# Optimization experiments

Measured on AMD Instinct MI355X. Metric: run time of the kernel, lower is better.

The kernel has to match this reference:

```python
import jax, jax.numpy as jnp
import numpy as np

HIDDEN = 2048
Q_HEADS = 16
KV_HEADS = 4
HEAD_DIM = HIDDEN // Q_HEADS  # 128
GROUPS = Q_HEADS // KV_HEADS  # 4


def setup_inputs() -> dict:
    key = jax.random.key(0)
    ks = jax.random.split(key, 5)
    scale = 1.0 / np.sqrt(HIDDEN)
    x = jax.random.normal(ks[0], (1, 4096, HIDDEN), dtype=jnp.float32)
    # nn.Linear weights stored as [out_features, in_features]
    Wq = jax.random.uniform(ks[1], (Q_HEADS * HEAD_DIM, HIDDEN), jnp.float32, -scale, scale)
    Wk = jax.random.uniform(ks[2], (KV_HEADS * HEAD_DIM, HIDDEN), jnp.float32, -scale, scale)
    Wv = jax.random.uniform(ks[3], (KV_HEADS * HEAD_DIM, HIDDEN), jnp.float32, -scale, scale)
    Wo = jax.random.uniform(ks[4], (HIDDEN, HIDDEN), jnp.float32, -scale, scale)
    return {"x": x, "Wq": Wq, "Wk": Wk, "Wv": Wv, "Wo": Wo}


def reference(x, Wq, Wk, Wv, Wo):
    b, s, _ = x.shape
    norm = jnp.asarray(np.sqrt(HEAD_DIM), x.dtype)
    # Projections (Linear without bias: x @ W.T)
    q = (x @ Wq.T).reshape(b, s, KV_HEADS, GROUPS, HEAD_DIM)  # group q heads by shared kv head
    k = (x @ Wk.T).reshape(b, s, KV_HEADS, HEAD_DIM)
    v = (x @ Wv.T).reshape(b, s, KV_HEADS, HEAD_DIM)
    # Scores: repeat_interleave of KV is equivalent to sharing k across the g axis
    att = jnp.einsum('bskgd,btkd->bkgst', q, k) / norm  # [b,kv,groups,s,s]
    att = jax.nn.softmax(att, axis=-1)
    out = jnp.einsum('bkgst,btkd->bskgd', att, v).reshape(b, s, HIDDEN)
    return out @ Wo.T
```

## Files before the change

kernel.cpp:

```cpp
#include <hip/hip_runtime.h>
#include <stdint.h>

#define SEQ 4096
#define HID 2048

typedef __attribute__((ext_vector_type(8))) short short8;
typedef __attribute__((ext_vector_type(4))) float f32x4;
typedef __attribute__((ext_vector_type(16))) float f32x16;
typedef unsigned int u32;
typedef __attribute__((ext_vector_type(4))) u32 u32x4;

__device__ __forceinline__ short bf16_rne(float f) {
  u32 u = __builtin_bit_cast(u32, f);
  u += 0x7FFFu + ((u >> 16) & 1u);
  return (short)(u >> 16);
}

__device__ __forceinline__ void gload16(const void* gp, void* lp) {
  __builtin_amdgcn_global_load_lds(
      (const __attribute__((address_space(1))) u32*)(uintptr_t)gp,
      (__attribute__((address_space(3))) u32*)(uintptr_t)lp, 16, 0, 0);
}

__global__ __launch_bounds__(256) void cast_bf16(const float* __restrict__ in,
                                                 short* __restrict__ out, int n8,
                                                 float scale) {
  int i = blockIdx.x * 256 + threadIdx.x;
  if (i >= n8) return;
  const f32x4* p = (const f32x4*)in + (size_t)i * 2;
  f32x4 a = p[0], b = p[1];
  short8 o;
#pragma unroll
  for (int j = 0; j < 4; ++j) { o[j] = bf16_rne(a[j] * scale); o[j + 4] = bf16_rne(b[j] * scale); }
  *((short8*)out + i) = o;
}

__global__ __launch_bounds__(256) void transpose_v(const short* __restrict__ qkv,
                                                   short* __restrict__ vt) {
  __shared__ __align__(16) short tile[64][72];
  int rb = blockIdx.x * 64, cb = blockIdx.y * 64;
  int tid = threadIdx.x;
  int tr = tid >> 3, tc = (tid & 7) * 8;
#pragma unroll
  for (int i = 0; i < 2; ++i)
    *(short8*)&tile[tr + i * 32][tc] =
        *(const short8*)&qkv[(size_t)(rb + tr + i * 32) * 3072 + 2560 + cb + tc];
  __syncthreads();
#pragma unroll
  for (int i = 0; i < 2; ++i) {
    int c = tr + i * 32;
    short8 v;
#pragma unroll
    for (int j = 0; j < 8; ++j) {
      int pos = tc + j;
      int tl = (pos & ~15) | (pos & 3) | ((pos & 4) << 1) | ((pos & 8) >> 1);
      v[j] = tile[tl][c];
    }
    *(short8*)&vt[(size_t)(cb + c) * SEQ + rb + tc] = v;
  }
}

template <typename CT>
__global__ __launch_bounds__(256, 2) void gemm_nt(const short* __restrict__ A,
                                                  const short* __restrict__ B,
                                                  CT* __restrict__ C, int M, int N, int K) {
  __shared__ __align__(16) short As[128 * 32];
  __shared__ __align__(16) short Bs[128 * 32];
  int tid = threadIdx.x, wave = tid >> 6, lane = tid & 63;
  int lr = lane & 15, lg = lane >> 4;
  int wr = wave >> 1, wc = wave & 1;
  size_t rowA0 = (size_t)blockIdx.y * 128, colB0 = (size_t)blockIdx.x * 128;
  f32x4 acc[4][4] = {};

  for (int kt = 0; kt < K; kt += 32) {
#pragma unroll
    for (int c = 0; c < 2; ++c) {
      int chunk = wave * 2 + c;
      int row = chunk * 16 + (lane >> 2);
      int col = (lane & 3) * 8;
      gload16(A + (rowA0 + row) * (size_t)K + kt + col, &As[chunk * 512]);
      gload16(B + (colB0 + row) * (size_t)K + kt + col, &Bs[chunk * 512]);
    }
    __syncthreads();
    short8 a[4], b[4];
#pragma unroll
    for (int i = 0; i < 4; ++i) {
      a[i] = *(const short8*)&As[(wr * 64 + i * 16 + lr) * 32 + lg * 8];
      b[i] = *(const short8*)&Bs[(wc * 64 + i * 16 + lr) * 32 + lg * 8];
    }
#pragma unroll
    for (int i = 0; i < 4; ++i)
#pragma unroll
      for (int j = 0; j < 4; ++j)
        acc[i][j] = __builtin_amdgcn_mfma_f32_16x16x32_bf16(a[i], b[j], acc[i][j], 0, 0, 0);
    __syncthreads();
  }
#pragma unroll
  for (int i = 0; i < 4; ++i)
#pragma unroll
    for (int j = 0; j < 4; ++j)
#pragma unroll
      for (int r = 0; r < 4; ++r) {
        size_t row = rowA0 + wr * 64 + i * 16 + lg * 4 + r;
        size_t col = colB0 + wc * 64 + j * 16 + lr;
        if constexpr (sizeof(CT) == 2) C[row * N + col] = (CT)bf16_rne(acc[i][j][r]);
        else C[row * N + col] = acc[i][j][r];
      }
}

__global__ __launch_bounds__(256, 2) void attn_kernel(const short* __restrict__ QKV,
                                                      const short* __restrict__ Vt,
                                                      short* __restrict__ Oat) {
  __shared__ __align__(16) short Ks[2][4096];
  __shared__ __align__(16) short Vs[2][4096];
  int tid = threadIdx.x, wave = tid >> 6, lane = tid & 63;
  int l31 = lane & 31, hi = lane >> 5;
  int h = blockIdx.y, kv = h >> 2;
  int q0 = blockIdx.x * 128 + wave * 32;

  short8 qf[8];
#pragma unroll
  for (int kb = 0; kb < 8; ++kb)
    qf[kb] = *(const short8*)&QKV[(size_t)(q0 + l31) * 3072 + h * 128 + kb * 16 + hi * 8];

  f32x16 oacc[4] = {};
  float lsum = 0.f;

  const short* Kbase = QKV + 2048 + kv * 128;

  auto stageK = [&](int b, int t0) {
#pragma unroll
    for (int cc = 0; cc < 2; ++cc) {
      int c = wave * 2 + cc;
      gload16(Kbase + (size_t)(t0 + l31) * 3072 + c * 16 + hi * 8, &Ks[b][c * 512]);
    }
  };
  auto stageV = [&](int b, int t0) {
#pragma unroll
    for (int cc = 0; cc < 2; ++cc) {
      int c = wave * 2 + cc;
      int d = (c & 1) * 64 + lane;
      gload16(Vt + (size_t)(kv * 128 + d) * SEQ + t0 + (c >> 1) * 8, &Vs[b][c * 512]);
    }
  };

  stageK(0, 0);
  stageV(0, 0);
  __syncthreads();
  int buf = 0;

  for (int t0 = 0; t0 < SEQ; t0 += 32) {
    int tn = (t0 + 32 < SEQ) ? t0 + 32 : 0;
    stageK(buf ^ 1, tn);
    stageV(buf ^ 1, tn);

    f32x16 sacc = {};
    __builtin_amdgcn_s_setprio(1);
#pragma unroll
    for (int kb = 0; kb < 8; ++kb) {
      short8 kf = *(const short8*)&Ks[buf][((kb * 2 + hi) * 32 + l31) * 8];
      sacc = __builtin_amdgcn_mfma_f32_32x32x16_bf16(kf, qf[kb], sacc, 0, 0, 0);
    }
    __builtin_amdgcn_s_setprio(0);

    float ps = 0.f;
    u32 w[8];
#pragma unroll
    for (int i = 0; i < 8; ++i) {
      float p0 = __builtin_amdgcn_exp2f(sacc[2 * i]);
      float p1 = __builtin_amdgcn_exp2f(sacc[2 * i + 1]);
      ps += p0 + p1;
      asm("v_cvt_pk_bf16_f32 %0, %1, %2" : "=v"(w[i]) : "v"(p0), "v"(p1));
    }
    lsum += ps;
    short8 pa0 = __builtin_bit_cast(short8, (u32x4){w[0], w[1], w[2], w[3]});
    short8 pa1 = __builtin_bit_cast(short8, (u32x4){w[4], w[5], w[6], w[7]});

    __builtin_amdgcn_s_setprio(1);
#pragma unroll
    for (int nb = 0; nb < 4; ++nb) {
      short8 v0 = *(const short8*)&Vs[buf][((hi)*128 + nb * 32 + l31) * 8];
      oacc[nb] = __builtin_amdgcn_mfma_f32_32x32x16_bf16(pa0, v0, oacc[nb], 0, 0, 0);
      short8 v1 = *(const short8*)&Vs[buf][((2 + hi) * 128 + nb * 32 + l31) * 8];
      oacc[nb] = __builtin_amdgcn_mfma_f32_32x32x16_bf16(pa1, v1, oacc[nb], 0, 0, 0);
    }
    __builtin_amdgcn_s_setprio(0);

    __syncthreads();
    buf ^= 1;
  }

  lsum += __shfl_xor(lsum, 32);
  float linv = 1.f / lsum;
#pragma unroll
  for (int r = 0; r < 16; ++r) {
    int qrow = (r & 3) + 8 * (r >> 2) + 4 * hi;
    float lr_ = __shfl(linv, qrow);
#pragma unroll
    for (int nb = 0; nb < 4; ++nb)
      Oat[(size_t)(q0 + qrow) * HID + h * 128 + nb * 32 + l31] = bf16_rne(oacc[nb][r] * lr_);
  }
}

extern "C" void kernel_launch(void* const* d_in, const int* in_sizes, int n_in,
                              void* d_out, int out_size, void* d_ws, size_t ws_size,
                              hipStream_t stream) {
  const float* x = (const float*)d_in[0];
  const float* Wq = (const float*)d_in[1];
  const float* Wk = (const float*)d_in[2];
  const float* Wv = (const float*)d_in[3];
  const float* Wo = (const float*)d_in[4];
  float* out = (float*)d_out;
  char* ws = (char*)d_ws;

  short* xb = (short*)(ws);
  short* wqkv = (short*)(ws + (16u << 20));
  short* wob = (short*)(ws + (28u << 20));
  short* qkv = (short*)(ws + (36u << 20));
  short* vt = wqkv;
  short* oat = xb;

  const float QSCALE = 0.12753102964551932f;

  cast_bf16<<<4096, 256, 0, stream>>>(x, xb, 1048576, 1.0f);
  cast_bf16<<<2048, 256, 0, stream>>>(Wq, wqkv, 524288, QSCALE);
  cast_bf16<<<512, 256, 0, stream>>>(Wk, wqkv + (size_t)2048 * 2048, 131072, 1.0f);
  cast_bf16<<<512, 256, 0, stream>>>(Wv, wqkv + (size_t)2560 * 2048, 131072, 1.0f);
  cast_bf16<<<2048, 256, 0, stream>>>(Wo, wob, 524288, 1.0f);

  gemm_nt<short><<<dim3(24, 32), 256, 0, stream>>>(xb, wqkv, qkv, 4096, 3072, 2048);
  transpose_v<<<dim3(64, 8), 256, 0, stream>>>(qkv, vt);
  attn_kernel<<<dim3(32, 16), 256, 0, stream>>>(qkv, vt, oat);
  gemm_nt<float><<<dim3(16, 32), 256, 0, stream>>>(oat, wob, out, 4096, HID, 2048);
}
```

Measured before the change: 278.8 us.

## Deepen attention K/V prefetch to a 4-buffer ring with partial vmcnt waits

Replaces the double-buffered K/V staging in the attention kernel with a four-slot ring that keeps loads two tiles ahead. Each iteration waits with s_waitcnt vmcnt(8) so only the oldest tile must have arrived, followed by a single raw s_barrier instead of a full __syncthreads at the end. The aim is to hide global-to-LDS latency behind the MFMA work. LDS use doubles to 64KB per block, which may lower occupancy from the two blocks per CU the launch bounds target. The single-barrier scheme depends on the ring depth to avoid overwriting a slot another wave is still reading.

```diff
diff --git a/kernel.cpp b/kernel.cpp
--- a/kernel.cpp
+++ b/kernel.cpp
@@ -111,8 +111,8 @@
 __global__ __launch_bounds__(256, 2) void attn_kernel(const short* __restrict__ QKV,
                                                       const short* __restrict__ Vt,
                                                       short* __restrict__ Oat) {
-  __shared__ __align__(16) short Ks[2][4096];
-  __shared__ __align__(16) short Vs[2][4096];
+  __shared__ __align__(16) short Ks[4][4096];
+  __shared__ __align__(16) short Vs[4][4096];
   int tid = threadIdx.x, wave = tid >> 6, lane = tid & 63;
   int l31 = lane & 31, hi = lane >> 5;
   int h = blockIdx.y, kv = h >> 2;
@@ -144,21 +144,30 @@
     }
   };
 
-  stageK(0, 0);
-  stageV(0, 0);
+  const int NT = SEQ / 32;
+
+  stageK(0, 0); stageV(0, 0);
+  stageK(1, 32); stageV(1, 32);
   __syncthreads();
-  int buf = 0;
-
-  for (int t0 = 0; t0 < SEQ; t0 += 32) {
-    int tn = (t0 + 32 < SEQ) ? t0 + 32 : 0;
-    stageK(buf ^ 1, tn);
-    stageV(buf ^ 1, tn);
+
+  for (int i = 0; i < NT; ++i) {
+    int ti = (i + 2 < NT) ? i + 2 : NT - 1;
+    int sb = (i + 2) & 3;
+    stageK(sb, ti * 32);
+    stageV(sb, ti * 32);
+
+    asm volatile("s_waitcnt vmcnt(8)" ::: "memory");
+    __builtin_amdgcn_sched_barrier(0);
+    __builtin_amdgcn_s_barrier();
+    __builtin_amdgcn_sched_barrier(0);
+
+    const int cb = i & 3;
 
     f32x16 sacc = {};
     __builtin_amdgcn_s_setprio(1);
 #pragma unroll
     for (int kb = 0; kb < 8; ++kb) {
-      short8 kf = *(const short8*)&Ks[buf][((kb * 2 + hi) * 32 + l31) * 8];
+      short8 kf = *(const short8*)&Ks[cb][((kb * 2 + hi) * 32 + l31) * 8];
       sacc = __builtin_amdgcn_mfma_f32_32x32x16_bf16(kf, qf[kb], sacc, 0, 0, 0);
     }
     __builtin_amdgcn_s_setprio(0);
@@ -166,11 +175,11 @@
     float ps = 0.f;
     u32 w[8];
 #pragma unroll
-    for (int i = 0; i < 8; ++i) {
-      float p0 = __builtin_amdgcn_exp2f(sacc[2 * i]);
-      float p1 = __builtin_amdgcn_exp2f(sacc[2 * i + 1]);
+    for (int ii = 0; ii < 8; ++ii) {
+      float p0 = __builtin_amdgcn_exp2f(sacc[2 * ii]);
+      float p1 = __builtin_amdgcn_exp2f(sacc[2 * ii + 1]);
       ps += p0 + p1;
-      asm("v_cvt_pk_bf16_f32 %0, %1, %2" : "=v"(w[i]) : "v"(p0), "v"(p1));
+      asm("v_cvt_pk_bf16_f32 %0, %1, %2" : "=v"(w[ii]) : "v"(p0), "v"(p1));
     }
     lsum += ps;
     short8 pa0 = __builtin_bit_cast(short8, (u32x4){w[0], w[1], w[2], w[3]});
@@ -179,15 +188,12 @@
     __builtin_amdgcn_s_setprio(1);
 #pragma unroll
     for (int nb = 0; nb < 4; ++nb) {
-      short8 v0 = *(const short8*)&Vs[buf][((hi)*128 + nb * 32 + l31) * 8];
+      short8 v0 = *(const short8*)&Vs[cb][((hi)*128 + nb * 32 + l31) * 8];
       oacc[nb] = __builtin_amdgcn_mfma_f32_32x32x16_bf16(pa0, v0, oacc[nb], 0, 0, 0);
-      short8 v1 = *(const short8*)&Vs[buf][((2 + hi) * 128 + nb * 32 + l31) * 8];
+      short8 v1 = *(const short8*)&Vs[cb][((2 + hi) * 128 + nb * 32 + l31) * 8];
       oacc[nb] = __builtin_amdgcn_mfma_f32_32x32x16_bf16(pa1, v1, oacc[nb], 0, 0, 0);
     }
     __builtin_amdgcn_s_setprio(0);
-
-    __syncthreads();
-    buf ^= 1;
   }
 
   lsum += __shfl_xor(lsum, 32);
```

Result: no change. 281.4 us (+0.9%).
